# Optimization experiments

Hardware: AMD Instinct MI355X
Metric: run time of the kernel (lower is better)

## Reference

```python
import jax, jax.numpy as jnp
import numpy as np

N_NODES = 50000
N_EDGES = 800000
N_GRAPHS = 64
EMB_DIM = 24
N_KERNELS = 2
M_DIM = 64
FOURIER = 4
POS_DIM = 3
EDGE_IN = 2 * FOURIER + 1 + 2 * EMB_DIM  # 57
MLP_DIM = 256
N_OUT = 4
FFNN_IN = EMB_DIM * (N_KERNELS + 1)  # 72


def _lin(key, fan_in, fan_out, stack=None):
    # xavier-uniform weight, zero bias (matches weights_init)
    lim = (6.0 / (fan_in + fan_out)) ** 0.5
    shp = ((stack,) if stack else ()) + (fan_in, fan_out)
    w = jax.random.uniform(key, shp, minval=-lim, maxval=lim, dtype=jnp.float32)
    b = jnp.zeros(((stack,) if stack else ()) + (fan_out,), jnp.float32)
    return w, b


def setup_inputs() -> dict:
    key = jax.random.key(0)
    ks = jax.random.split(key, 20)
    z = jax.random.randint(ks[0], (N_NODES,), 0, 22)
    pos = jax.random.normal(ks[1], (N_NODES, POS_DIM), jnp.float32)
    edge_index = jax.random.randint(ks[2], (2, N_EDGES), 0, N_NODES)
    batch_idx = jnp.sort(jax.random.randint(ks[3], (N_NODES,), 0, N_GRAPHS))
    lim_e = (6.0 / (22 + EMB_DIM)) ** 0.5
    emb_table = jax.random.uniform(ks[4], (22, EMB_DIM), minval=-lim_e, maxval=lim_e, dtype=jnp.float32)
    emb_w, emb_b = _lin(ks[5], EMB_DIM, EMB_DIM)
    # EGNN kernel params, stacked over N_KERNELS
    ew1, eb1 = _lin(ks[6], EDGE_IN, EDGE_IN * 2, N_KERNELS)
    ew2, eb2 = _lin(ks[7], EDGE_IN * 2, M_DIM, N_KERNELS)
    cw1, cb1 = _lin(ks[8], M_DIM, M_DIM * 4, N_KERNELS)
    cw2, cb2 = _lin(ks[9], M_DIM * 4, 1, N_KERNELS)
    nw1, nb1 = _lin(ks[10], EMB_DIM + M_DIM, EMB_DIM * 2, N_KERNELS)
    nw2, nb2 = _lin(ks[11], EMB_DIM * 2, EMB_DIM, N_KERNELS)
    # ffnn: Linear(72,256), Linear(256,256), Linear(256,256), Linear(256,4)
    f0w, f0b = _lin(ks[12], FFNN_IN, MLP_DIM)
    f1w, f1b = _lin(ks[13], MLP_DIM, MLP_DIM)
    f2w, f2b = _lin(ks[14], MLP_DIM, MLP_DIM)
    fow, fob = _lin(ks[15], MLP_DIM, N_OUT)
    return dict(z=z, pos=pos, edge_index=edge_index, batch_idx=batch_idx,
                emb_table=emb_table, emb_w=emb_w, emb_b=emb_b,
                ew1=ew1, eb1=eb1, ew2=ew2, eb2=eb2,
                cw1=cw1, cb1=cb1, cw2=cw2, cb2=cb2,
                nw1=nw1, nb1=nb1, nw2=nw2, nb2=nb2,
                f0w=f0w, f0b=f0b, f1w=f1w, f1b=f1b, f2w=f2w, f2b=f2b,
                fow=fow, fob=fob)


def _egnn_layer(feats, coors, src, dst, ew1, eb1, ew2, eb2, cw1, cb1, cw2, cb2, nw1, nb1, nw2, nb2):
    # EGNN_sparse (PyG flow source_to_target: i=dst=edge_index[1], j=src=edge_index[0])
    rel = coors[src] - coors[dst]                       # [E,3]
    d = jnp.sum(rel * rel, axis=-1, keepdims=True)      # [E,1] squared distance
    scales = 2.0 ** jnp.arange(FOURIER, dtype=feats.dtype)
    ds = d / scales                                     # [E,4]
    edge_feat = jnp.concatenate([jnp.sin(ds), jnp.cos(ds), d], axis=-1)  # [E,9]
    e_in = jnp.concatenate([feats[dst], feats[src], edge_feat], axis=-1)  # [E,57]
    m_ij = jax.nn.silu(jax.nn.silu(e_in @ ew1 + eb1) @ ew2 + eb2)         # [E,64]
    coor_w = jax.nn.silu(m_ij @ cw1 + cb1) @ cw2 + cb2                    # [E,1]
    coors_out = coors + jax.ops.segment_sum(coor_w * rel, dst, num_segments=N_NODES)
    m_i = jax.ops.segment_sum(m_ij, dst, num_segments=N_NODES)            # [N,64]
    h = jax.nn.silu(jnp.concatenate([feats, m_i], axis=-1) @ nw1 + nb1)
    feats_out = feats + (h @ nw2 + nb2)
    return feats_out, coors_out


def reference(z, pos, edge_index, batch_idx, emb_table, emb_w, emb_b,
              ew1, eb1, ew2, eb2, cw1, cb1, cw2, cb2, nw1, nb1, nw2, nb2,
              f0w, f0b, f1w, f1b, f2w, f2b, fow, fob):
    src, dst = edge_index[0], edge_index[1]
    feats = emb_table[z] @ emb_w + emb_b
    coors = pos
    flist = [feats]
    for k in range(N_KERNELS):
        feats, coors = _egnn_layer(feats, coors, src, dst,
                                   ew1[k], eb1[k], ew2[k], eb2[k],
                                   cw1[k], cb1[k], cw2[k], cb2[k],
                                   nw1[k], nb1[k], nw2[k], nb2[k])
        flist.append(feats)
    x = jax.nn.silu(jnp.concatenate(flist, axis=-1))     # [N,72]
    x = jax.nn.silu(x @ f0w + f0b)
    x = jax.nn.silu(x @ f1w + f1b)
    x = jax.nn.silu(x @ f2w + f2b)                       # [N,256]
    cnt = jax.ops.segment_sum(jnp.ones((x.shape[0],), x.dtype), batch_idx, num_segments=N_GRAPHS)
    pooled = jax.ops.segment_sum(x, batch_idx, num_segments=N_GRAPHS) / jnp.maximum(cnt, 1.0)[:, None]
    return jax.nn.sigmoid(pooled @ fow + fob)            # [B,4]
```

## Files before the change

### kernel.cpp

```cpp
#include <hip/hip_runtime.h>
#include <hip/hip_bf16.h>

#define N_NODES  50000
#define N_EDGES  800000
#define N_GRAPHS 64
#define EMB      24
#define MDIM     64
#define EDGE_IN  57
#define EH       114
#define CH       256
#define NIN      88
#define NH       48
#define MLP      256
#define ETILE    128
#define NTILE    64

typedef __bf16 bf16_t;
typedef __bf16 bf16x8 __attribute__((ext_vector_type(8)));
typedef __bf16 bf16x4 __attribute__((ext_vector_type(4)));
typedef float  f32x4  __attribute__((ext_vector_type(4)));

__device__ __forceinline__ float siluf(float x) {
    return x * __builtin_amdgcn_rcpf(1.0f + __expf(-x));
}

__device__ __forceinline__ f32x4 silu4(f32x4 x) {
    f32x4 t = x * (-1.44269504088896341f);
    f32x4 e;
    e[0] = __builtin_amdgcn_exp2f(t[0]);
    e[1] = __builtin_amdgcn_exp2f(t[1]);
    e[2] = __builtin_amdgcn_exp2f(t[2]);
    e[3] = __builtin_amdgcn_exp2f(t[3]);
    f32x4 den = e + 1.0f;
    f32x4 r;
    r[0] = __builtin_amdgcn_rcpf(den[0]);
    r[1] = __builtin_amdgcn_rcpf(den[1]);
    r[2] = __builtin_amdgcn_rcpf(den[2]);
    r[3] = __builtin_amdgcn_rcpf(den[3]);
    return x * r;
}

__global__ void embed_kernel(const int* __restrict__ z, const float* __restrict__ table,
                             const float* __restrict__ w, const float* __restrict__ b,
                             const int* __restrict__ batch, float* __restrict__ f0,
                             bf16_t* __restrict__ fb0, float* __restrict__ cnt)
{
    int n = blockIdx.x * blockDim.x + threadIdx.x;
    if (n >= N_NODES) return;
    float r[EMB];
    const float4* tr = reinterpret_cast<const float4*>(table + z[n] * EMB);
    #pragma unroll
    for (int q = 0; q < 6; q++) {
        float4 v = tr[q];
        r[q*4] = v.x; r[q*4+1] = v.y; r[q*4+2] = v.z; r[q*4+3] = v.w;
    }
    float o[EMB];
    #pragma unroll
    for (int j = 0; j < EMB; j++) o[j] = b[j];
    #pragma unroll
    for (int i = 0; i < EMB; i++) {
        #pragma unroll
        for (int j = 0; j < EMB; j++) o[j] = fmaf(r[i], w[i*EMB + j], o[j]);
    }
    float4* dst = reinterpret_cast<float4*>(f0 + (size_t)n * EMB);
    #pragma unroll
    for (int q = 0; q < 6; q++) dst[q] = make_float4(o[q*4], o[q*4+1], o[q*4+2], o[q*4+3]);
    bf16x8* bdst = reinterpret_cast<bf16x8*>(fb0 + (size_t)n * EMB);
    #pragma unroll
    for (int q = 0; q < 3; q++) {
        bf16x8 pk;
        #pragma unroll
        for (int j = 0; j < 8; j++) pk[j] = (bf16_t)o[q*8 + j];
        bdst[q] = pk;
    }
    atomicAdd(&cnt[batch[n]], 1.0f);
}

#define PK_W1   (128*64)
#define PK_W2   (64*128)
#define PK_CW   (256*64)
#define PK_F0   (256*128)
#define PK_FM   (256*256)
#define PK_TOT  (2*PK_W1 + 2*PK_W2 + PK_CW + PK_F0 + 2*PK_FM)
__global__ void pack_kernel(const float* __restrict__ ew1, const float* __restrict__ eb1,
                            const float* __restrict__ ew2, const float* __restrict__ eb2,
                            const float* __restrict__ cw1, const float* __restrict__ f0w,
                            const float* __restrict__ f1w, const float* __restrict__ f2w,
                            bf16_t* __restrict__ pw)
{
    int idx = blockIdx.x * blockDim.x + threadIdx.x;
    if (idx >= PK_TOT) return;
    float v = 0.0f;
    if (idx < 2 * PK_W1) {
        int l = idx / PK_W1, r = idx - l * PK_W1;
        int n = r >> 6, k = r & 63;
        if (n < EH && k < EDGE_IN)       v = ew1[(l * EDGE_IN + k) * EH + n];
        else if (n < EH && k == EDGE_IN) v = eb1[l * EH + n];
    } else if (idx < 2 * PK_W1 + 2 * PK_W2) {
        int r0 = idx - 2 * PK_W1;
        int l = r0 / PK_W2, r = r0 - l * PK_W2;
        int n = r >> 7, k = r & 127;
        if (k < EH)       v = ew2[(l * EH + k) * MDIM + n];
        else if (k == EH) v = eb2[l * MDIM + n];
    } else if (idx < 2 * PK_W1 + 2 * PK_W2 + PK_CW) {
        int r = idx - (2 * PK_W1 + 2 * PK_W2);
        int n = r >> 6, k = r & 63;
        v = cw1[k * CH + n];
    } else if (idx < 2 * PK_W1 + 2 * PK_W2 + PK_CW + PK_F0) {
        int r = idx - (2 * PK_W1 + 2 * PK_W2 + PK_CW);
        int n = r >> 7, k = r & 127;
        if (k < 72) v = f0w[k * MLP + n];
    } else {
        int r0 = idx - (2 * PK_W1 + 2 * PK_W2 + PK_CW + PK_F0);
        int l = r0 / PK_FM, r = r0 - l * PK_FM;
        int n = r >> 8, k = r & 255;
        v = (l == 0) ? f1w[k * MLP + n] : f2w[k * MLP + n];
    }
    pw[idx] = (bf16_t)v;
}

__global__ void hist_kernel(const int* __restrict__ dst, int* __restrict__ deg)
{
    int e = blockIdx.x * blockDim.x + threadIdx.x;
    if (e < N_EDGES) atomicAdd(&deg[dst[e]], 1);
}

__global__ __launch_bounds__(1024)
void scan_kernel(const int* __restrict__ deg, int* __restrict__ cursor)
{
    __shared__ int part[1024];
    int t = threadIdx.x;
    const int PER = 49;
    int base = t * PER;
    int s = 0;
    for (int i = 0; i < PER; i++) {
        int p = base + i;
        if (p < N_NODES) s += deg[p];
    }
    part[t] = s;
    __syncthreads();
    for (int off = 1; off < 1024; off <<= 1) {
        int add = (t >= off) ? part[t - off] : 0;
        __syncthreads();
        part[t] += add;
        __syncthreads();
    }
    int run = (t > 0) ? part[t - 1] : 0;
    for (int i = 0; i < PER; i++) {
        int p = base + i;
        if (p < N_NODES) { cursor[p] = run; run += deg[p]; }
    }
}

__global__ void scatter_kernel(const int* __restrict__ src, const int* __restrict__ dst,
                               int* __restrict__ cursor, int* __restrict__ srcs_s,
                               int* __restrict__ dsts_s)
{
    int e = blockIdx.x * blockDim.x + threadIdx.x;
    if (e >= N_EDGES) return;
    int d = dst[e];
    int pos = atomicAdd(&cursor[d], 1);
    srcs_s[pos] = src[e];
    dsts_s[pos] = d;
}

template<int COOR>
__global__ __launch_bounds__(256, 4)
void edge_mfma(const bf16_t* __restrict__ fb, const float* __restrict__ coors,
               const int* __restrict__ srcs_s, const int* __restrict__ dsts_s,
               const bf16_t* __restrict__ W1t, const bf16_t* __restrict__ W2t,
               const bf16_t* __restrict__ CW1t, const float* __restrict__ cb1,
               const float* __restrict__ cw2, const float* __restrict__ cb2,
               float* __restrict__ m_i, float* __restrict__ cdelta)
{
    __shared__ __align__(16) char R1raw[4 * 8192];
    __shared__ float s_rel[COOR ? ETILE * 3 : 4];
    __shared__ float s_cacc[COOR ? ETILE : 4];
    __shared__ int   s_dst[ETILE];

    const int t = threadIdx.x;
    const int w = t >> 6;
    const int l = t & 63;
    const int row0 = w * 32;
    const int ebase = blockIdx.x * ETILE;
    const int l15 = l & 15, l4 = l >> 4;
    bf16_t* slab16 = (bf16_t*)(R1raw + w * 8192);
    float*  slab32 = (float*) (R1raw + w * 8192);

    bf16x8 w1f0[8];
    #pragma unroll
    for (int ft = 0; ft < 8; ft++)
        w1f0[ft] = *(const bf16x8*)&W1t[(ft*16 + l15)*64 + l4*8];

    {
        int e_loc = t >> 1, half = t & 1;
        int e_l = e_loc & 31;
        int e = ebase + e_loc;
        int s = srcs_s[e], d = dsts_s[e];
        if (half == 0) {
            s_dst[e_loc] = d;
            const bf16x8* fp = reinterpret_cast<const bf16x8*>(fb + (size_t)d * EMB);
            #pragma unroll
            for (int g = 0; g < 3; g++)
                *(bf16x8*)&slab16[e_l*64 + (g ^ (e_l & 7))*8] = fp[g];
        } else {
            const bf16x8* fp = reinterpret_cast<const bf16x8*>(fb + (size_t)s * EMB);
            #pragma unroll
            for (int g = 0; g < 3; g++)
                *(bf16x8*)&slab16[e_l*64 + ((g + 3) ^ (e_l & 7))*8] = fp[g];
            float rx = coors[s*3+0] - coors[d*3+0];
            float ry = coors[s*3+1] - coors[d*3+1];
            float rz = coors[s*3+2] - coors[d*3+2];
            float d2 = rx*rx + ry*ry + rz*rz;
            if (COOR) { s_rel[e_loc*3+0] = rx; s_rel[e_loc*3+1] = ry; s_rel[e_loc*3+2] = rz; }
            bf16x8 p6, p7;
            p6[0]=(bf16_t)__sinf(d2);        p6[1]=(bf16_t)__sinf(d2*0.5f);
            p6[2]=(bf16_t)__sinf(d2*0.25f);  p6[3]=(bf16_t)__sinf(d2*0.125f);
            p6[4]=(bf16_t)__cosf(d2);        p6[5]=(bf16_t)__cosf(d2*0.5f);
            p6[6]=(bf16_t)__cosf(d2*0.25f);  p6[7]=(bf16_t)__cosf(d2*0.125f);
            p7[0]=(bf16_t)d2; p7[1]=(bf16_t)1.0f;
            p7[2]=(bf16_t)0.f; p7[3]=(bf16_t)0.f; p7[4]=(bf16_t)0.f;
            p7[5]=(bf16_t)0.f; p7[6]=(bf16_t)0.f; p7[7]=(bf16_t)0.f;
            *(bf16x8*)&slab16[e_l*64 + (6 ^ (e_l & 7))*8] = p6;
            *(bf16x8*)&slab16[e_l*64 + (7 ^ (e_l & 7))*8] = p7;
        }
    }

    f32x4 acc1[2][8];
    #pragma unroll
    for (int et = 0; et < 2; et++)
        #pragma unroll
        for (int ft = 0; ft < 8; ft++) acc1[et][ft] = (f32x4){0.f,0.f,0.f,0.f};
    __builtin_amdgcn_s_setprio(1);
    #pragma unroll
    for (int ks = 0; ks < 2; ks++) {
        bf16x8 bfrag[2];
        #pragma unroll
        for (int et = 0; et < 2; et++) {
            int e_l = et*16 + l15;
            bfrag[et] = *(const bf16x8*)&slab16[e_l*64 + ((ks*4 + l4) ^ (e_l & 7))*8];
        }
        #pragma unroll
        for (int ft = 0; ft < 8; ft++) {
            bf16x8 a = ks ? *(const bf16x8*)&W1t[(ft*16 + l15)*64 + (4 + l4)*8] : w1f0[ft];
            acc1[0][ft] = __builtin_amdgcn_mfma_f32_16x16x32_bf16(a, bfrag[0], acc1[0][ft], 0, 0, 0);
            acc1[1][ft] = __builtin_amdgcn_mfma_f32_16x16x32_bf16(a, bfrag[1], acc1[1][ft], 0, 0, 0);
        }
    }
    __builtin_amdgcn_s_setprio(0);
    #pragma unroll
    for (int et = 0; et < 2; et++)
        #pragma unroll
        for (int ft = 0; ft < 8; ft++) {
            int e_l = et*16 + l15;
            int f0 = ft*16 + l4*4;
            f32x4 hv = silu4(acc1[et][ft]);
            if (f0 == EH - 2) hv[2] = 1.0f;
            bf16x4 pk;
            #pragma unroll
            for (int r4 = 0; r4 < 4; r4++) pk[r4] = (bf16_t)hv[r4];
            *(bf16x4*)&slab16[e_l*128 + ((f0 >> 3) ^ (e_l & 7))*8 + (f0 & 7)] = pk;
        }

    f32x4 acc2[2][4];
    #pragma unroll
    for (int et = 0; et < 2; et++)
        #pragma unroll
        for (int ft = 0; ft < 4; ft++) acc2[et][ft] = (f32x4){0.f,0.f,0.f,0.f};
    __builtin_amdgcn_s_setprio(1);
    #pragma unroll
    for (int ks = 0; ks < 4; ks++) {
        bf16x8 bfrag[2];
        #pragma unroll
        for (int et = 0; et < 2; et++) {
            int e_l = et*16 + l15;
            bfrag[et] = *(const bf16x8*)&slab16[e_l*128 + ((ks*4 + l4) ^ (e_l & 7))*8];
        }
        #pragma unroll
        for (int ft = 0; ft < 4; ft++) {
            bf16x8 a = *(const bf16x8*)&W2t[(ft*16 + l15)*128 + (ks*4 + l4)*8];
            acc2[0][ft] = __builtin_amdgcn_mfma_f32_16x16x32_bf16(a, bfrag[0], acc2[0][ft], 0, 0, 0);
            acc2[1][ft] = __builtin_amdgcn_mfma_f32_16x16x32_bf16(a, bfrag[1], acc2[1][ft], 0, 0, 0);
        }
    }
    __builtin_amdgcn_s_setprio(0);
    #pragma unroll
    for (int et = 0; et < 2; et++)
        #pragma unroll
        for (int ft = 0; ft < 4; ft++) {
            int e_l = et*16 + l15;
            int f0 = ft*16 + l4*4;
            f32x4 v = silu4(acc2[et][ft]);
            *(f32x4*)&slab32[e_l*64 + (((f0 >> 2) ^ (e_l & 7)) << 2)] = v;
        }

    {
        int col = l;
        int gsw_base = col >> 2, cw = col & 3;
        int cur = s_dst[row0];
        float run = 0.f;
        for (int i = 0; i < 32; i++) {
            int d = s_dst[row0 + i];
            float v = slab32[i*64 + ((gsw_base ^ (i & 7)) << 2) + cw];
            if (d != cur) { atomicAdd(&m_i[(size_t)cur*64 + col], run); run = 0.f; cur = d; }
            run += v;
        }
        atomicAdd(&m_i[(size_t)cur*64 + col], run);
    }

    if (COOR) {
        f32x4 csumv0 = (f32x4){0.f,0.f,0.f,0.f};
        f32x4 csumv1 = (f32x4){0.f,0.f,0.f,0.f};
        #pragma unroll
        for (int half = 0; half < 2; half++) {
            f32x4 acc3[2][8];
            #pragma unroll
            for (int et = 0; et < 2; et++)
                #pragma unroll
                for (int ft = 0; ft < 8; ft++) acc3[et][ft] = (f32x4){0.f,0.f,0.f,0.f};
            __builtin_amdgcn_s_setprio(1);
            #pragma unroll
            for (int ks = 0; ks < 2; ks++) {
                bf16x8 bfrag[2];
                #pragma unroll
                for (int et = 0; et < 2; et++) {
                    int e_l = et*16 + l15;
                    int g0 = (ks*4 + l4) * 2;
                    f32x4 lo = *(const f32x4*)&slab32[e_l*64 + ((g0 ^ (e_l & 7)) << 2)];
                    f32x4 hi = *(const f32x4*)&slab32[e_l*64 + (((g0 + 1) ^ (e_l & 7)) << 2)];
                    bf16x8 bk;
                    #pragma unroll
                    for (int j = 0; j < 4; j++) { bk[j] = (bf16_t)lo[j]; bk[j+4] = (bf16_t)hi[j]; }
                    bfrag[et] = bk;
                }
                #pragma unroll
                for (int ft = 0; ft < 8; ft++) {
                    bf16x8 a = *(const bf16x8*)&CW1t[(half*128 + ft*16 + l15)*64 + (ks*4 + l4)*8];
                    acc3[0][ft] = __builtin_amdgcn_mfma_f32_16x16x32_bf16(a, bfrag[0], acc3[0][ft], 0, 0, 0);
                    acc3[1][ft] = __builtin_amdgcn_mfma_f32_16x16x32_bf16(a, bfrag[1], acc3[1][ft], 0, 0, 0);
                }
            }
            __builtin_amdgcn_s_setprio(0);
            #pragma unroll
            for (int ft = 0; ft < 8; ft++) {
                int f0 = half*128 + ft*16 + l4*4;
                f32x4 c1 = *(const f32x4*)&cb1[f0];
                f32x4 w2 = *(const f32x4*)&cw2[f0];
                csumv0 += silu4(acc3[0][ft] + c1) * w2;
                csumv1 += silu4(acc3[1][ft] + c1) * w2;
            }
        }
        float csum0 = (csumv0[0] + csumv0[1]) + (csumv0[2] + csumv0[3]);
        float csum1 = (csumv1[0] + csumv1[1]) + (csumv1[2] + csumv1[3]);
        csum0 += __shfl_xor(csum0, 16);
        csum0 += __shfl_xor(csum0, 32);
        csum1 += __shfl_xor(csum1, 16);
        csum1 += __shfl_xor(csum1, 32);
        float cb2v = cb2[0];
        if (l < 32) {
            s_cacc[row0 + l] = ((l & 16) ? csum1 : csum0) + cb2v;
        }
        if (l < 32) {
            int row = row0 + l;
            int d = s_dst[row];
            bool head = (l == 0) || (s_dst[row - 1] != d);
            if (head) {
                float ax = 0.f, ay = 0.f, az = 0.f;
                int i = l;
                do {
                    int r = row0 + i;
                    float c = s_cacc[r];
                    ax = fmaf(c, s_rel[r*3+0], ax);
                    ay = fmaf(c, s_rel[r*3+1], ay);
                    az = fmaf(c, s_rel[r*3+2], az);
                    ++i;
                } while (i < 32 && s_dst[row0 + i] == d);
                atomicAdd(&cdelta[d*3+0], ax);
                atomicAdd(&cdelta[d*3+1], ay);
                atomicAdd(&cdelta[d*3+2], az);
            }
        }
    }
}

template<int EMIT_BF16>
__global__ __launch_bounds__(256)
void node_kernel(const float* __restrict__ feats, const float* __restrict__ m_i,
                 const float* __restrict__ nw1, const float* __restrict__ nb1,
                 const float* __restrict__ nw2, const float* __restrict__ nb2,
                 float* __restrict__ fout, bf16_t* __restrict__ fbout)
{
    __shared__ float s_w1t[NH * NIN];
    __shared__ float s_b1[NH];
    __shared__ float s_w2[NH * EMB];
    __shared__ float s_b2[EMB];
    const int tid = threadIdx.x;
    for (int idx = tid; idx < NH * NIN; idx += 256) {
        int k = idx / NIN, i = idx - k * NIN;
        s_w1t[idx] = nw1[i * NH + k];
    }
    for (int idx = tid; idx < NH * EMB; idx += 256) s_w2[idx] = nw2[idx];
    if (tid < NH) s_b1[tid] = nb1[tid];
    if (tid < EMB) s_b2[tid] = nb2[tid];
    __syncthreads();

    int n = blockIdx.x * 256 + tid;
    if (n >= N_NODES) return;

    float in[NIN];
    const float4* fp = reinterpret_cast<const float4*>(feats + (size_t)n * EMB);
    #pragma unroll
    for (int q = 0; q < 6; q++) {
        float4 v = fp[q];
        in[q*4] = v.x; in[q*4+1] = v.y; in[q*4+2] = v.z; in[q*4+3] = v.w;
    }
    const float4* mp = reinterpret_cast<const float4*>(m_i + (size_t)n * MDIM);
    #pragma unroll
    for (int q = 0; q < 16; q++) {
        float4 v = mp[q];
        in[EMB+q*4] = v.x; in[EMB+q*4+1] = v.y; in[EMB+q*4+2] = v.z; in[EMB+q*4+3] = v.w;
    }
    float o[EMB];
    #pragma unroll
    for (int j = 0; j < EMB; j++) o[j] = in[j] + s_b2[j];
    for (int k = 0; k < NH; k++) {
        const float* w1 = &s_w1t[k * NIN];
        float a0 = 0.f, a1 = 0.f, a2 = 0.f, a3 = 0.f;
        #pragma unroll
        for (int i = 0; i < NIN; i += 4) {
            a0 = fmaf(in[i],   w1[i],   a0);
            a1 = fmaf(in[i+1], w1[i+1], a1);
            a2 = fmaf(in[i+2], w1[i+2], a2);
            a3 = fmaf(in[i+3], w1[i+3], a3);
        }
        float h = siluf(s_b1[k] + ((a0 + a1) + (a2 + a3)));
        const float* w2 = &s_w2[k * EMB];
        #pragma unroll
        for (int j = 0; j < EMB; j++) o[j] = fmaf(h, w2[j], o[j]);
    }
    float4* dst = reinterpret_cast<float4*>(fout + (size_t)n * EMB);
    #pragma unroll
    for (int q = 0; q < 6; q++) dst[q] = make_float4(o[q*4], o[q*4+1], o[q*4+2], o[q*4+3]);
    if (EMIT_BF16) {
        bf16x8* bdst = reinterpret_cast<bf16x8*>(fbout + (size_t)n * EMB);
        #pragma unroll
        for (int q = 0; q < 3; q++) {
            bf16x8 pk;
            #pragma unroll
            for (int j = 0; j < 8; j++) pk[j] = (bf16_t)o[q*8 + j];
            bdst[q] = pk;
        }
    }
}

__global__ void coor_kernel(const float* __restrict__ pos, const float* __restrict__ cdelta,
                            float* __restrict__ out)
{
    int i = blockIdx.x * blockDim.x + threadIdx.x;
    if (i < N_NODES * 3) out[i] = pos[i] + cdelta[i];
}

__global__ __launch_bounds__(512, 4)
void ffnn_fused(const float* __restrict__ f0, const float* __restrict__ f1,
                const float* __restrict__ f2,
                const bf16_t* __restrict__ W0p, const bf16_t* __restrict__ W1p,
                const bf16_t* __restrict__ W2p,
                const float* __restrict__ b0, const float* __restrict__ b1,
                const float* __restrict__ b2,
                const int* __restrict__ batch, float* __restrict__ pooled)
{
    __shared__ __align__(16) bf16_t sH[NTILE * 256];
    __shared__ int s_batch[NTILE];
    const int t = threadIdx.x;
    const int w = t >> 6, l = t & 63;
    const int l15 = l & 15, q = l >> 4;
    const int mt = w & 3;
    const int nh = w >> 2;
    const int mrow0 = mt * 16;
    const int n0 = blockIdx.x * NTILE;

    {
        int row = t >> 3, part = t & 7;
        int n = n0 + row;
        bool valid = n < N_NODES;
        if (part == 7) s_batch[row] = valid ? batch[n] : -1;
        #pragma unroll
        for (int gi = 0; gi < 2; gi++) {
            int g = part * 2 + gi;
            bf16x8 pk;
            #pragma unroll
            for (int j = 0; j < 8; j++) pk[j] = (bf16_t)0.f;
            if (valid && g < 9) {
                const float* sp = (g < 3) ? f0 + (size_t)n*EMB + 8*g
                                : (g < 6) ? f1 + (size_t)n*EMB + 8*(g-3)
                                          : f2 + (size_t)n*EMB + 8*(g-6);
                float4 a = ((const float4*)sp)[0], b = ((const float4*)sp)[1];
                f32x4 sa = silu4((f32x4){a.x, a.y, a.z, a.w});
                f32x4 sb = silu4((f32x4){b.x, b.y, b.z, b.w});
                pk[0]=(bf16_t)sa[0]; pk[1]=(bf16_t)sa[1]; pk[2]=(bf16_t)sa[2]; pk[3]=(bf16_t)sa[3];
                pk[4]=(bf16_t)sb[0]; pk[5]=(bf16_t)sb[1]; pk[6]=(bf16_t)sb[2]; pk[7]=(bf16_t)sb[3];
            }
            *(bf16x8*)&sH[row*128 + (g ^ (row & 7))*8] = pk;
        }
    }
    __syncthreads();

    bf16x8 a0[4];
    {
        int r = mrow0 + l15;
        #pragma unroll
        for (int ks = 0; ks < 4; ks++)
            a0[ks] = *(const bf16x8*)&sH[r*128 + ((ks*4 + q) ^ (r & 7))*8];
    }
    __syncthreads();

    f32x4 acc[8];
    #pragma unroll
    for (int nt = 0; nt < 8; nt++) {
        float bv = b0[(nh*8 + nt)*16 + l15];
        acc[nt] = (f32x4){bv, bv, bv, bv};
    }
    #pragma unroll
    for (int ks = 0; ks < 4; ks++)
        #pragma unroll
        for (int nt = 0; nt < 8; nt++) {
            int n = (nh*8 + nt)*16 + l15;
            bf16x8 b = *(const bf16x8*)&W0p[n*128 + (ks*4 + q)*8];
            acc[nt] = __builtin_amdgcn_mfma_f32_16x16x32_bf16(a0[ks], b, acc[nt], 0, 0, 0);
        }
    #pragma unroll
    for (int nt = 0; nt < 8; nt++) {
        f32x4 sv = silu4(acc[nt]);
        #pragma unroll
        for (int r4 = 0; r4 < 4; r4++) {
            int row = mrow0 + q*4 + r4;
            int col = (nh*8 + nt)*16 + l15;
            sH[row*256 + ((col >> 3) ^ (row & 7))*8 + (col & 7)] = (bf16_t)sv[r4];
        }
    }
    __syncthreads();

    #pragma unroll
    for (int layer = 0; layer < 2; layer++) {
        const bf16_t* Wp = layer ? W2p : W1p;
        const float*  bb = layer ? b2  : b1;
        #pragma unroll
        for (int nt = 0; nt < 8; nt++) {
            float bv = bb[(nh*8 + nt)*16 + l15];
            acc[nt] = (f32x4){bv, bv, bv, bv};
        }
        for (int ks = 0; ks < 8; ks++) {
            int r = mrow0 + l15;
            bf16x8 a = *(const bf16x8*)&sH[r*256 + ((ks*4 + q) ^ (r & 7))*8];
            #pragma unroll
            for (int nt = 0; nt < 8; nt++) {
                int n = (nh*8 + nt)*16 + l15;
                bf16x8 b = *(const bf16x8*)&Wp[n*256 + (ks*4 + q)*8];
                acc[nt] = __builtin_amdgcn_mfma_f32_16x16x32_bf16(a, b, acc[nt], 0, 0, 0);
            }
        }
        __syncthreads();
        #pragma unroll
        for (int nt = 0; nt < 8; nt++) {
            f32x4 sv = silu4(acc[nt]);
            #pragma unroll
            for (int r4 = 0; r4 < 4; r4++) {
                int row = mrow0 + q*4 + r4;
                int col = (nh*8 + nt)*16 + l15;
                sH[row*256 + ((col >> 3) ^ (row & 7))*8 + (col & 7)] = (bf16_t)sv[r4];
            }
        }
        __syncthreads();
    }

    {
        int j = t & 255;
        int rh = t >> 8;
        int g = j >> 3, jo = j & 7;
        int cur = -1;
        float run = 0.f;
        for (int i = rh*32; i < rh*32 + 32; i++) {
            int bb = s_batch[i];
            if (bb != cur) {
                if (cur >= 0) atomicAdd(&pooled[cur * MLP + j], run);
                run = 0.f; cur = bb;
            }
            if (bb >= 0) run += (float)sH[i*256 + (g ^ (i & 7))*8 + jo];
        }
        if (cur >= 0) atomicAdd(&pooled[cur * MLP + j], run);
    }
}

__global__ void final_kernel(const float* __restrict__ pooled, const float* __restrict__ cnt,
                             const float* __restrict__ fow, const float* __restrict__ fob,
                             float* __restrict__ out)
{
    int t = threadIdx.x;
    int bg = t >> 2, o = t & 3;
    float c = fmaxf(cnt[bg], 1.0f);
    float acc = 0.f;
    for (int i = 0; i < MLP; i++) acc = fmaf(pooled[bg * MLP + i], fow[i * 4 + o], acc);
    acc = acc / c + fob[o];
    out[t] = 1.0f / (1.0f + __expf(-acc));
}

extern "C" void kernel_launch(void* const* d_in, const int* in_sizes, int n_in,
                              void* d_out, int out_size, void* d_ws, size_t ws_size,
                              hipStream_t stream)
{
    const int*   z     = (const int*)  d_in[0];
    const float* pos   = (const float*)d_in[1];
    const int*   eidx  = (const int*)  d_in[2];
    const int*   batch = (const int*)  d_in[3];
    const float* embt  = (const float*)d_in[4];
    const float* embw  = (const float*)d_in[5];
    const float* embb  = (const float*)d_in[6];
    const float* ew1   = (const float*)d_in[7];
    const float* eb1   = (const float*)d_in[8];
    const float* ew2   = (const float*)d_in[9];
    const float* eb2   = (const float*)d_in[10];
    const float* cw1   = (const float*)d_in[11];
    const float* cb1   = (const float*)d_in[12];
    const float* cw2   = (const float*)d_in[13];
    const float* cb2   = (const float*)d_in[14];
    const float* nw1   = (const float*)d_in[15];
    const float* nb1   = (const float*)d_in[16];
    const float* nw2   = (const float*)d_in[17];
    const float* nb2   = (const float*)d_in[18];
    const float* f0w   = (const float*)d_in[19];
    const float* f0b   = (const float*)d_in[20];
    const float* f1w   = (const float*)d_in[21];
    const float* f1b   = (const float*)d_in[22];
    const float* f2w   = (const float*)d_in[23];
    const float* f2b   = (const float*)d_in[24];
    const float* fow   = (const float*)d_in[25];
    const float* fob   = (const float*)d_in[26];

    float* ws     = (float*)d_ws;
    float* f0     = ws;
    float* f1v    = f0 + (size_t)N_NODES * EMB;
    float* f2v    = f1v + (size_t)N_NODES * EMB;
    bf16_t* fb0   = (bf16_t*)(f2v + (size_t)N_NODES * EMB);
    bf16_t* fb1   = fb0 + (size_t)N_NODES * EMB;
    float* coorsA = (float*)(fb1 + (size_t)N_NODES * EMB);
    float* cdelta = coorsA + N_NODES * 3;
    float* m_i    = cdelta + N_NODES * 3;
    float* pooled = m_i + (size_t)N_NODES * MDIM;
    float* cnt    = pooled + N_GRAPHS * MLP;
    int*   deg    = (int*)(cnt + N_GRAPHS);
    int*   cursor = deg + N_NODES;
    int*   srcs_s = cursor + N_NODES;
    int*   dsts_s = srcs_s + N_EDGES;
    bf16_t* packw = (bf16_t*)(dsts_s + N_EDGES);
    bf16_t* W1t0  = packw;
    bf16_t* W1t1  = W1t0 + PK_W1;
    bf16_t* W2t0  = W1t1 + PK_W1;
    bf16_t* W2t1  = W2t0 + PK_W2;
    bf16_t* CW1t  = W2t1 + PK_W2;
    bf16_t* W0p   = CW1t + PK_CW;
    bf16_t* W1p   = W0p + PK_F0;
    bf16_t* W2p   = W1p + PK_FM;

    hipMemsetAsync(cdelta, 0, N_NODES * 3 * sizeof(float), stream);
    hipMemsetAsync(m_i, 0, (size_t)N_NODES * MDIM * sizeof(float), stream);
    hipMemsetAsync(pooled, 0, (N_GRAPHS * MLP + N_GRAPHS) * sizeof(float), stream);
    hipMemsetAsync(deg, 0, N_NODES * sizeof(int), stream);

    const int* e_src = eidx;
    const int* e_dst = eidx + N_EDGES;
    pack_kernel<<<(PK_TOT + 255) / 256, 256, 0, stream>>>(ew1, eb1, ew2, eb2, cw1,
                                                          f0w, f1w, f2w, packw);
    hist_kernel<<<(N_EDGES + 255) / 256, 256, 0, stream>>>(e_dst, deg);
    scan_kernel<<<1, 1024, 0, stream>>>(deg, cursor);
    scatter_kernel<<<(N_EDGES + 255) / 256, 256, 0, stream>>>(e_src, e_dst, cursor, srcs_s, dsts_s);

    embed_kernel<<<(N_NODES + 255) / 256, 256, 0, stream>>>(z, embt, embw, embb, batch, f0, fb0, cnt);

    const int EBLK = N_EDGES / ETILE;
    edge_mfma<1><<<EBLK, 256, 0, stream>>>(fb0, pos, srcs_s, dsts_s,
        W1t0, W2t0, CW1t, cb1, cw2, cb2, m_i, cdelta);
    node_kernel<1><<<(N_NODES + 255) / 256, 256, 0, stream>>>(f0, m_i, nw1, nb1, nw2, nb2, f1v, fb1);
    coor_kernel<<<(N_NODES * 3 + 255) / 256, 256, 0, stream>>>(pos, cdelta, coorsA);
    hipMemsetAsync(m_i, 0, (size_t)N_NODES * MDIM * sizeof(float), stream);
    edge_mfma<0><<<EBLK, 256, 0, stream>>>(fb1, coorsA, srcs_s, dsts_s,
        W1t1, W2t1, CW1t, cb1, cw2, cb2, m_i, nullptr);
    node_kernel<0><<<(N_NODES + 255) / 256, 256, 0, stream>>>(f1v, m_i,
        nw1 + NIN * NH, nb1 + NH, nw2 + NH * EMB, nb2 + EMB, f2v, nullptr);

    const int FBLK = (N_NODES + NTILE - 1) / NTILE;
    ffnn_fused<<<FBLK, 512, 0, stream>>>(f0, f1v, f2v, W0p, W1p, W2p,
                                         f0b, f1b, f2b, batch, pooled);

    final_kernel<<<1, 256, 0, stream>>>(pooled, cnt, fow, fob, (float*)d_out);
}
```

Measured before the change: 963.9 us.

## Feed MFMA B-fragments from registers by permuting packed weight K order

Reorders the K dimension of the packed W2 and CW1 weights so that MFMA accumulator outputs from the previous layer can be used directly as B operands in registers. This removes the LDS round-trip for the hidden layer and the fp32-to-bf16 reload for the coordinate MLP input. It also drops the preloaded W1 fragment cache to save registers. The cost is more live registers for the held fragments, and correctness depends on the permutation matching the MFMA lane layout.

```diff
diff --git a/kernel.cpp b/kernel.cpp
--- a/kernel.cpp
+++ b/kernel.cpp
@@ -40,6 +40,13 @@
     return x * r;
 }
 
+__device__ __forceinline__ bf16x8 cat44(bf16x4 a, bf16x4 b) {
+    bf16x8 r;
+    r[0]=a[0]; r[1]=a[1]; r[2]=a[2]; r[3]=a[3];
+    r[4]=b[0]; r[5]=b[1]; r[6]=b[2]; r[7]=b[3];
+    return r;
+}
+
 __global__ void embed_kernel(const int* __restrict__ z, const float* __restrict__ table,
                              const float* __restrict__ w, const float* __restrict__ b,
                              const int* __restrict__ batch, float* __restrict__ f0,
@@ -99,13 +106,17 @@
     } else if (idx < 2 * PK_W1 + 2 * PK_W2) {
         int r0 = idx - 2 * PK_W1;
         int l = r0 / PK_W2, r = r0 - l * PK_W2;
-        int n = r >> 7, k = r & 127;
-        if (k < EH)       v = ew2[(l * EH + k) * MDIM + n];
-        else if (k == EH) v = eb2[l * MDIM + n];
+        int n = r >> 7, kp = r & 127;
+        int ks = kp >> 5, g = (kp >> 3) & 3, j = kp & 7;
+        int f = 16 * (2*ks + (j >> 2)) + 4*g + (j & 3);
+        if (f < EH)       v = ew2[(l * EH + f) * MDIM + n];
+        else if (f == EH) v = eb2[l * MDIM + n];
     } else if (idx < 2 * PK_W1 + 2 * PK_W2 + PK_CW) {
         int r = idx - (2 * PK_W1 + 2 * PK_W2);
-        int n = r >> 6, k = r & 63;
-        v = cw1[k * CH + n];
+        int n = r >> 6, kp = r & 63;
+        int ks = kp >> 5, g = (kp >> 3) & 3, j = kp & 7;
+        int f = 16 * (2*ks + (j >> 2)) + 4*g + (j & 3);
+        v = cw1[f * CH + n];
     } else if (idx < 2 * PK_W1 + 2 * PK_W2 + PK_CW + PK_F0) {
         int r = idx - (2 * PK_W1 + 2 * PK_W2 + PK_CW);
         int n = r >> 7, k = r & 127;
@@ -186,11 +197,6 @@
     const int l15 = l & 15, l4 = l >> 4;
     bf16_t* slab16 = (bf16_t*)(R1raw + w * 8192);
     float*  slab32 = (float*) (R1raw + w * 8192);
-
-    bf16x8 w1f0[8];
-    #pragma unroll
-    for (int ft = 0; ft < 8; ft++)
-        w1f0[ft] = *(const bf16x8*)&W1t[(ft*16 + l15)*64 + l4*8];
 
     {
         int e_loc = t >> 1, half = t & 1;
@@ -242,24 +248,24 @@
         }
         #pragma unroll
         for (int ft = 0; ft < 8; ft++) {
-            bf16x8 a = ks ? *(const bf16x8*)&W1t[(ft*16 + l15)*64 + (4 + l4)*8] : w1f0[ft];
+            bf16x8 a = *(const bf16x8*)&W1t[(ft*16 + l15)*64 + (ks*4 + l4)*8];
             acc1[0][ft] = __builtin_amdgcn_mfma_f32_16x16x32_bf16(a, bfrag[0], acc1[0][ft], 0, 0, 0);
             acc1[1][ft] = __builtin_amdgcn_mfma_f32_16x16x32_bf16(a, bfrag[1], acc1[1][ft], 0, 0, 0);
         }
     }
     __builtin_amdgcn_s_setprio(0);
+
+    bf16x4 h1b[2][8];
     #pragma unroll
     for (int et = 0; et < 2; et++)
         #pragma unroll
         for (int ft = 0; ft < 8; ft++) {
-            int e_l = et*16 + l15;
-            int f0 = ft*16 + l4*4;
             f32x4 hv = silu4(acc1[et][ft]);
-            if (f0 == EH - 2) hv[2] = 1.0f;
+            if (ft == 7 && l4 == 0) hv[2] = 1.0f;
             bf16x4 pk;
             #pragma unroll
             for (int r4 = 0; r4 < 4; r4++) pk[r4] = (bf16_t)hv[r4];
-            *(bf16x4*)&slab16[e_l*128 + ((f0 >> 3) ^ (e_l & 7))*8 + (f0 & 7)] = pk;
+            h1b[et][ft] = pk;
         }
 
     f32x4 acc2[2][4];
@@ -270,28 +276,32 @@
     __builtin_amdgcn_s_setprio(1);
     #pragma unroll
     for (int ks = 0; ks < 4; ks++) {
-        bf16x8 bfrag[2];
-        #pragma unroll
-        for (int et = 0; et < 2; et++) {
-            int e_l = et*16 + l15;
-            bfrag[et] = *(const bf16x8*)&slab16[e_l*128 + ((ks*4 + l4) ^ (e_l & 7))*8];
-        }
+        bf16x8 bfrag0 = cat44(h1b[0][2*ks], h1b[0][2*ks+1]);
+        bf16x8 bfrag1 = cat44(h1b[1][2*ks], h1b[1][2*ks+1]);
         #pragma unroll
         for (int ft = 0; ft < 4; ft++) {
             bf16x8 a = *(const bf16x8*)&W2t[(ft*16 + l15)*128 + (ks*4 + l4)*8];
-            acc2[0][ft] = __builtin_amdgcn_mfma_f32_16x16x32_bf16(a, bfrag[0], acc2[0][ft], 0, 0, 0);
-            acc2[1][ft] = __builtin_amdgcn_mfma_f32_16x16x32_bf16(a, bfrag[1], acc2[1][ft], 0, 0, 0);
+            acc2[0][ft] = __builtin_amdgcn_mfma_f32_16x16x32_bf16(a, bfrag0, acc2[0][ft], 0, 0, 0);
+            acc2[1][ft] = __builtin_amdgcn_mfma_f32_16x16x32_bf16(a, bfrag1, acc2[1][ft], 0, 0, 0);
         }
     }
     __builtin_amdgcn_s_setprio(0);
+
+    bf16x4 mb[2][4];
     #pragma unroll
     for (int et = 0; et < 2; et++)
         #pragma unroll
         for (int ft = 0; ft < 4; ft++) {
             int e_l = et*16 + l15;
             int f0 = ft*16 + l4*4;
-            f32x4 v = silu4(acc2[et][ft]);
-            *(f32x4*)&slab32[e_l*64 + (((f0 >> 2) ^ (e_l & 7)) << 2)] = v;
+            f32x4 mv = silu4(acc2[et][ft]);
+            *(f32x4*)&slab32[e_l*64 + (((f0 >> 2) ^ (e_l & 7)) << 2)] = mv;
+            if (COOR) {
+                bf16x4 pk;
+                #pragma unroll
+                for (int r4 = 0; r4 < 4; r4++) pk[r4] = (bf16_t)mv[r4];
+                mb[et][ft] = pk;
+            }
         }
 
     {
@@ -321,23 +331,13 @@
             __builtin_amdgcn_s_setprio(1);
             #pragma unroll
             for (int ks = 0; ks < 2; ks++) {
-                bf16x8 bfrag[2];
-                #pragma unroll
-                for (int et = 0; et < 2; et++) {
-                    int e_l = et*16 + l15;
-                    int g0 = (ks*4 + l4) * 2;
-                    f32x4 lo = *(const f32x4*)&slab32[e_l*64 + ((g0 ^ (e_l & 7)) << 2)];
-                    f32x4 hi = *(const f32x4*)&slab32[e_l*64 + (((g0 + 1) ^ (e_l & 7)) << 2)];
-                    bf16x8 bk;
-                    #pragma unroll
-                    for (int j = 0; j < 4; j++) { bk[j] = (bf16_t)lo[j]; bk[j+4] = (bf16_t)hi[j]; }
-                    bfrag[et] = bk;
-                }
+                bf16x8 bfrag0 = cat44(mb[0][2*ks], mb[0][2*ks+1]);
+                bf16x8 bfrag1 = cat44(mb[1][2*ks], mb[1][2*ks+1]);
                 #pragma unroll
                 for (int ft = 0; ft < 8; ft++) {
                     bf16x8 a = *(const bf16x8*)&CW1t[(half*128 + ft*16 + l15)*64 + (ks*4 + l4)*8];
-                    acc3[0][ft] = __builtin_amdgcn_mfma_f32_16x16x32_bf16(a, bfrag[0], acc3[0][ft], 0, 0, 0);
-                    acc3[1][ft] = __builtin_amdgcn_mfma_f32_16x16x32_bf16(a, bfrag[1], acc3[1][ft], 0, 0, 0);
+                    acc3[0][ft] = __builtin_amdgcn_mfma_f32_16x16x32_bf16(a, bfrag0, acc3[0][ft], 0, 0, 0);
+                    acc3[1][ft] = __builtin_amdgcn_mfma_f32_16x16x32_bf16(a, bfrag1, acc3[1][ft], 0, 0, 0);
                 }
             }
             __builtin_amdgcn_s_setprio(0);
```

After: 960.8 us (median of 3 runs). About the same (-0.3%).
